# Kernel tuning notes

Measured on AMD Instinct MI355X. Metric: run time of the kernel, lower is better.

Reference implementation:

```python
import jax, jax.numpy as jnp
import numpy as np

N_NODES = 100000
N_EDGES = 3200000
IN_DIM, H_DIM, OUT_DIM = 512, 256, 128
NEG_SLOPE = 0.25


def setup_inputs() -> dict:
    key = jax.random.key(0)
    ks = jax.random.split(key, 8)
    x = jax.random.normal(ks[0], (N_NODES, IN_DIM), dtype=jnp.float32)
    # xavier-normal-ish init for weights, zero bias (matches module init)
    W1 = jax.random.normal(ks[1], (IN_DIM, H_DIM), dtype=jnp.float32) * np.sqrt(2.0 / (IN_DIM + H_DIM))
    b1 = jnp.zeros((H_DIM,), dtype=jnp.float32)
    W2 = jax.random.normal(ks[2], (H_DIM, OUT_DIM), dtype=jnp.float32) * np.sqrt(2.0 / (H_DIM + OUT_DIM))
    b2 = jnp.zeros((OUT_DIM,), dtype=jnp.float32)
    adj_row = jax.random.randint(ks[3], (N_EDGES,), 0, N_NODES, dtype=jnp.int32)
    adj_col = jax.random.randint(ks[4], (N_EDGES,), 0, N_NODES, dtype=jnp.int32)
    # positive normalized-ish edge weights (like D^-1/2 A D^-1/2 entries)
    edge_weight = jax.random.uniform(ks[5], (N_EDGES,), dtype=jnp.float32) * 0.05
    return {"x": x, "W1": W1, "b1": b1, "W2": W2, "b2": b2,
            "adj_row": adj_row, "adj_col": adj_col, "edge_weight": edge_weight}


def reference(x, W1, b1, W2, b2, adj_row, adj_col, edge_weight):
    n = x.shape[0]

    def spmm(support):
        # out[r] = sum over edges (r, c): w * support[c]   (COO SpMM)
        msgs = edge_weight[:, None] * support[adj_col]  # [E, d] gather
        return jax.ops.segment_sum(msgs, adj_row, num_segments=n)

    def leaky(h):
        return jnp.where(h > 0, h, NEG_SLOPE * h)

    h = leaky(spmm(x @ W1) + b1)          # gc1 + leaky_relu (dropout = eval mode)
    h = leaky(spmm(h @ W2) + b2)          # gc2 + leaky_relu
    return h
```

## Files before the change

kernel.cpp:

```cpp
#include <hip/hip_runtime.h>

typedef unsigned short u16;
typedef unsigned char u8;
typedef __attribute__((ext_vector_type(8))) __bf16 bf16x8;
typedef __attribute__((ext_vector_type(4))) float f32x4;

#define CAP   4608
#define CAPO  5504
#define CHUNK 8192
#define NBKT_PAD 800

static __device__ __forceinline__ u16 f2bf(float f) {
    return __builtin_bit_cast(u16, (__bf16)f);
}
static __device__ __forceinline__ void gl_lds16(const void* g, void* l) {
    __builtin_amdgcn_global_load_lds((const __attribute__((address_space(1))) void*)g,
                                     (__attribute__((address_space(3))) void*)l, 16, 0, 0);
}


__global__ __launch_bounds__(256) void bucket_k(const int* __restrict__ row,
                                                const int* __restrict__ col,
                                                const float* __restrict__ w,
                                                int* __restrict__ gcount,
                                                int2* __restrict__ edges, int E) {
    __shared__ int hist[NBKT_PAD];
    __shared__ int lscan[NBKT_PAD];
    __shared__ int lcnt[NBKT_PAD];
    __shared__ int gbase[NBKT_PAD];
    __shared__ int tsum[256];
    __shared__ int2 pay[CHUNK];
    __shared__ int  dst[CHUNK];
    const int base = blockIdx.x * CHUNK;
    const int cntC = min(CHUNK, E - base);
    const int tid = threadIdx.x;

    for (int i = tid; i < NBKT_PAD; i += 256) { hist[i] = 0; lcnt[i] = 0; }
    __syncthreads();

    for (int i = tid; i < cntC; i += 256) atomicAdd(&hist[row[base + i] >> 7], 1);
    __syncthreads();

    int h[4], s = 0;
    #pragma unroll
    for (int j = 0; j < 4; ++j) {
        int bb = tid * 4 + j;
        h[j] = (bb < NBKT_PAD) ? hist[bb] : 0;
        s += h[j];
    }
    tsum[tid] = s;
    __syncthreads();
    for (int d = 1; d < 256; d <<= 1) {
        int t = (tid >= d) ? tsum[tid - d] : 0;
        __syncthreads();
        tsum[tid] += t;
        __syncthreads();
    }
    int run = tsum[tid] - s;
    #pragma unroll
    for (int j = 0; j < 4; ++j) {
        int bb = tid * 4 + j;
        if (bb < NBKT_PAD) {
            lscan[bb] = run;
            run += h[j];
            if (h[j] > 0) gbase[bb] = atomicAdd(&gcount[bb], h[j]);
        }
    }
    __syncthreads();

    for (int i = tid; i < cntC; i += 256) {
        int r = row[base + i];
        int c = col[base + i];
        float ww = w[base + i];
        int bb = r >> 7;
        int lp = atomicAdd(&lcnt[bb], 1);
        int slot = lscan[bb] + lp;
        int pos = gbase[bb] + lp;
        pay[slot] = make_int2(((r & 127) << 17) | c, __float_as_int(ww));
        dst[slot] = (pos < CAP) ? bb * CAP + pos : -1;
    }
    __syncthreads();

    for (int i = tid; i < cntC; i += 256) {
        int d = dst[i];
        if (d >= 0) edges[d] = pay[i];
    }
}


__global__ __launch_bounds__(256) void rsort_k(const int* __restrict__ gcount,
                                               const int2* __restrict__ edges,
                                               int* __restrict__ colsO,
                                               float* __restrict__ wO,
                                               int2* __restrict__ rc, int n, int nbkt) {
    __shared__ int hist[128];
    __shared__ int sbase[128];
    __shared__ int lcnt[128];
    __shared__ int sc[128];
    __shared__ int colsL[CAPO];
    __shared__ float wL[CAPO];
    const int b = blockIdx.x, tid = threadIdx.x;
    const int cnt = min(gcount[b], CAP);
    const int2* eb = edges + (size_t)b * CAP;

    if (tid < 128) { hist[tid] = 0; lcnt[tid] = 0; }
    for (int i = tid; i < CAPO; i += 256) { colsL[i] = 0; wL[i] = 0.f; }
    __syncthreads();

    for (int i = tid; i < cnt; i += 256) atomicAdd(&hist[((unsigned)eb[i].x) >> 17], 1);
    __syncthreads();

    int hp = 0;
    if (tid < 128) { hp = (hist[tid] + 7) & ~7; sc[tid] = hp; }
    __syncthreads();
    for (int d = 1; d < 128; d <<= 1) {
        int t = 0;
        if (tid < 128 && tid >= d) t = sc[tid - d];
        __syncthreads();
        if (tid < 128) sc[tid] += t;
        __syncthreads();
    }
    if (tid < 128) {
        int start = sc[tid] - hp;
        sbase[tid] = start;
        int gr = b * 128 + tid;
        if (gr < n) rc[gr] = make_int2(b * CAPO + start, hp);
    }
    __syncthreads();

    for (int i = tid; i < cnt; i += 256) {
        int2 e = eb[i];
        int rr = ((unsigned)e.x) >> 17;
        int slot = sbase[rr] + atomicAdd(&lcnt[rr], 1);
        colsL[slot] = (e.x & 0x1FFFF) << 8;
        wL[slot] = __int_as_float(e.y);
    }
    __syncthreads();

    int* co = colsO + (size_t)b * CAPO;
    float* wo = wO + (size_t)b * CAPO;
    for (int i = tid; i < CAPO; i += 256) { co[i] = colsL[i]; wo[i] = wL[i]; }
    if (b == nbkt - 1 && tid < 64) {
        colsO[(size_t)nbkt * CAPO + tid] = 0;
        wO[(size_t)nbkt * CAPO + tid] = 0.f;
    }
}


__global__ __launch_bounds__(256) void wscale_k(const int* __restrict__ cols,
                                                const float* __restrict__ wr,
                                                const float* __restrict__ scales,
                                                float* __restrict__ ws, int total) {
    int i = (blockIdx.x * 256 + threadIdx.x) * 4;
    const int stride = gridDim.x * 1024;
    for (; i < total; i += stride) {
        int4 c = *(const int4*)(cols + i);
        float4 w = *(const float4*)(wr + i);
        float4 o;
        o.x = w.x * scales[((unsigned)c.x) >> 8];
        o.y = w.y * scales[((unsigned)c.y) >> 8];
        o.z = w.z * scales[((unsigned)c.z) >> 8];
        o.w = w.w * scales[((unsigned)c.w) >> 8];
        *(float4*)(ws + i) = o;
    }
}


__global__ void transpose_w2(const float* __restrict__ W1, u16* __restrict__ W1T,
                             const float* __restrict__ W2, u16* __restrict__ W2T,
                             int* __restrict__ gcount) {
    const int T1 = 512 * 256;
    const int T2 = 256 * 128;
    int i = blockIdx.x * blockDim.x + threadIdx.x;
    if (i < NBKT_PAD) gcount[i] = 0;
    if (i < T1) {
        int k = i / 256, nn = i % 256;
        W1T[nn * 512 + k] = f2bf(W1[i]);
    } else if (i < T1 + T2) {
        int j = i - T1;
        int k = j / 128, nn = j % 128;
        W2T[nn * 256 + k] = f2bf(W2[j]);
    }
}


template <int K, int NWN, bool AF32>
__global__ void gemm_fq(const void* __restrict__ Ap,
                        const u16* __restrict__ BT,
                        u8* __restrict__ supq,
                        float* __restrict__ scales, int M) {
    constexpr int BN = NWN * 64;
    constexpr int THREADS = NWN * 128;
    constexpr int A_ISS = 8192 / (THREADS * 16);
    constexpr int B_ISS = (BN * 64) / (THREADS * 16);
    constexpr int LOGN = (NWN == 4) ? 2 : 1;
    static_assert(!AF32 || (4096 / (THREADS * 8)) == 1, "AF32 path assumes A_CH==1");
    __shared__ alignas(16) u16 As[128 * 32];
    __shared__ alignas(16) u16 Bs[BN * 32];
    __shared__ float rmax[128][NWN];
    __shared__ u8 qtile[128 * BN];

    const int tid = threadIdx.x;
    const int lane = tid & 63, wv = tid >> 6;
    const int wm = wv >> LOGN, wn = wv & (NWN - 1);
    const int lr = lane & 15, lg = lane >> 4;
    const int mblk = blockIdx.x;
    f32x4 acc[4][4] = {};
    const float* Af = (const float*)Ap;
    const u16* Ab = (const u16*)Ap;

    const u16* gB[B_ISS];
    u16* lB[B_ISS];
    #pragma unroll
    for (int i = 0; i < B_ISS; ++i) {
        int t8 = i * THREADS + tid;
        gB[i] = BT + (long)(t8 >> 2) * K + (t8 & 3) * 8;
        lB[i] = Bs + i * THREADS * 8 + wv * 512;
    }

    if constexpr (AF32) {
        long r = (long)mblk * 128 + (tid >> 2);
        if (r >= M) r = M - 1;
        const float* gAf0 = Af + r * K + (tid & 3) * 8;
        u16* lAf0 = As + (tid >> 2) * 32 + (tid & 3) * 8;

        float4 pf0 = *(const float4*)(gAf0 + 0);
        float4 pf1 = *(const float4*)(gAf0 + 4);
        #pragma unroll 4
        for (int kt = 0; kt < K; kt += 32) {
            #pragma unroll
            for (int i = 0; i < B_ISS; ++i) gl_lds16(gB[i] + kt, lB[i]);
            __builtin_amdgcn_sched_barrier(0);
            const int ktn = (kt + 32 < K) ? kt + 32 : 0;
            float4 nf0 = *(const float4*)(gAf0 + ktn);
            float4 nf1 = *(const float4*)(gAf0 + ktn + 4);
            bf16x8 t;
            t[0] = (__bf16)pf0.x; t[1] = (__bf16)pf0.y; t[2] = (__bf16)pf0.z; t[3] = (__bf16)pf0.w;
            t[4] = (__bf16)pf1.x; t[5] = (__bf16)pf1.y; t[6] = (__bf16)pf1.z; t[7] = (__bf16)pf1.w;
            *(bf16x8*)lAf0 = t;
            asm volatile("s_waitcnt vmcnt(2) lgkmcnt(0)" ::: "memory");
            __builtin_amdgcn_sched_barrier(0);
            __builtin_amdgcn_s_barrier();
            __builtin_amdgcn_sched_barrier(0);

            bf16x8 a[4], b[4];
            #pragma unroll
            for (int mi = 0; mi < 4; ++mi)
                a[mi] = *(const bf16x8*)&As[(wm * 64 + mi * 16 + lr) * 32 + lg * 8];
            #pragma unroll
            for (int ni = 0; ni < 4; ++ni)
                b[ni] = *(const bf16x8*)&Bs[(wn * 64 + ni * 16 + lr) * 32 + lg * 8];
            #pragma unroll
            for (int mi = 0; mi < 4; ++mi)
                #pragma unroll
                for (int ni = 0; ni < 4; ++ni)
                    acc[mi][ni] = __builtin_amdgcn_mfma_f32_16x16x32_bf16(a[mi], b[ni], acc[mi][ni], 0, 0, 0);
            __builtin_amdgcn_sched_barrier(0);
            __builtin_amdgcn_s_barrier();
            __builtin_amdgcn_sched_barrier(0);
            pf0 = nf0; pf1 = nf1;
        }
    } else {
        const u16* gA[A_ISS];
        u16* lA[A_ISS];
        #pragma unroll
        for (int i = 0; i < A_ISS; ++i) {
            int t8 = i * THREADS + tid;
            long r = (long)mblk * 128 + (t8 >> 2);
            if (r >= M) r = M - 1;
            gA[i] = Ab + r * K + (t8 & 3) * 8;
            lA[i] = As + i * THREADS * 8 + wv * 512;
        }
        #pragma unroll 2
        for (int kt = 0; kt < K; kt += 32) {
            #pragma unroll
            for (int i = 0; i < A_ISS; ++i) gl_lds16(gA[i] + kt, lA[i]);
            #pragma unroll
            for (int i = 0; i < B_ISS; ++i) gl_lds16(gB[i] + kt, lB[i]);
            __syncthreads();

            bf16x8 a[4], b[4];
            #pragma unroll
            for (int mi = 0; mi < 4; ++mi)
                a[mi] = *(const bf16x8*)&As[(wm * 64 + mi * 16 + lr) * 32 + lg * 8];
            #pragma unroll
            for (int ni = 0; ni < 4; ++ni)
                b[ni] = *(const bf16x8*)&Bs[(wn * 64 + ni * 16 + lr) * 32 + lg * 8];
            #pragma unroll
            for (int mi = 0; mi < 4; ++mi)
                #pragma unroll
                for (int ni = 0; ni < 4; ++ni)
                    acc[mi][ni] = __builtin_amdgcn_mfma_f32_16x16x32_bf16(a[mi], b[ni], acc[mi][ni], 0, 0, 0);
            __syncthreads();
        }
    }

    #pragma unroll
    for (int mi = 0; mi < 4; ++mi) {
        #pragma unroll
        for (int j = 0; j < 4; ++j) {
            float m = 0.f;
            #pragma unroll
            for (int ni = 0; ni < 4; ++ni) m = fmaxf(m, fabsf(acc[mi][ni][j]));
            m = fmaxf(m, __shfl_xor(m, 1));
            m = fmaxf(m, __shfl_xor(m, 2));
            m = fmaxf(m, __shfl_xor(m, 4));
            m = fmaxf(m, __shfl_xor(m, 8));
            if (lr == 0) rmax[wm * 64 + mi * 16 + lg * 4 + j][wn] = m;
        }
    }
    __syncthreads();

    #pragma unroll
    for (int mi = 0; mi < 4; ++mi) {
        #pragma unroll
        for (int j = 0; j < 4; ++j) {
            const int rl = wm * 64 + mi * 16 + lg * 4 + j;
            float m = rmax[rl][0];
            #pragma unroll
            for (int w2 = 1; w2 < NWN; ++w2) m = fmaxf(m, rmax[rl][w2]);
            const float inv = (m > 0.f) ? 127.f / m : 0.f;
            #pragma unroll
            for (int ni = 0; ni < 4; ++ni) {
                int q = (int)rintf(acc[mi][ni][j] * inv) + 128;
                qtile[rl * BN + wn * 64 + ni * 16 + lr] = (u8)q;
            }
        }
    }
    if (tid < 128) {
        int gr = mblk * 128 + tid;
        if (gr < M) {
            float m = rmax[tid][0];
            #pragma unroll
            for (int w2 = 1; w2 < NWN; ++w2) m = fmaxf(m, rmax[tid][w2]);
            scales[gr] = m * (1.f / 127.f);
        }
    }
    __syncthreads();

    constexpr int CHUNKS = (128 * BN) / (THREADS * 16);
    #pragma unroll
    for (int cc = 0; cc < CHUNKS; ++cc) {
        int off = cc * THREADS * 16 + tid * 16;
        int gr = mblk * 128 + off / BN;
        if (gr < M)
            *(int4*)(supq + (size_t)mblk * 128 * BN + off) = *(const int4*)&qtile[off];
    }
}


__global__ __launch_bounds__(256) void spmm_l1(const int2* __restrict__ rc,
                                               const int* __restrict__ cols,
                                               const float* __restrict__ ws,
                                               const u8* __restrict__ supq,
                                               const float* __restrict__ bias,
                                               u16* __restrict__ obf, int n) {
    const int r = blockIdx.x * 4 + (threadIdx.x >> 6);
    if (r >= n) return;
    const int lane = threadIdx.x & 63;
    const int half = lane >> 5;
    const unsigned lsub8 = (unsigned)(lane & 31) * 8;
    float acc[8] = {0.f, 0.f, 0.f, 0.f, 0.f, 0.f, 0.f, 0.f};
    float kk = 0.f;
    const int2 se = rc[r];
    const int e0  = __builtin_amdgcn_readfirstlane(se.x);
    const int cnt = __builtin_amdgcn_readfirstlane(se.y);
    const int* __restrict__ cp = cols + e0;
    const float* __restrict__ wp = ws + e0;

#define L1_ISSUE(G0, G1, G2, G3, IDX) {                                              \
    int4 ca = *(const int4*)(cp + (IDX));                                            \
    int4 cb = *(const int4*)(cp + (IDX) + 4);                                        \
    G0 = *(const uint2*)(supq + ((unsigned)(half ? ca.y : ca.x) + lsub8));           \
    G1 = *(const uint2*)(supq + ((unsigned)(half ? ca.w : ca.z) + lsub8));           \
    G2 = *(const uint2*)(supq + ((unsigned)(half ? cb.y : cb.x) + lsub8));           \
    G3 = *(const uint2*)(supq + ((unsigned)(half ? cb.w : cb.z) + lsub8)); }

#define L1_PAIR(WX, WY, G) {                                                         \
    const float wsel = half ? (WY) : (WX);                                           \
    kk += wsel;                                                                      \
    acc[0] += wsel * (float)((G).x & 0xFF);                                          \
    acc[1] += wsel * (float)(((G).x >> 8) & 0xFF);                                   \
    acc[2] += wsel * (float)(((G).x >> 16) & 0xFF);                                  \
    acc[3] += wsel * (float)((G).x >> 24);                                           \
    acc[4] += wsel * (float)((G).y & 0xFF);                                          \
    acc[5] += wsel * (float)(((G).y >> 8) & 0xFF);                                   \
    acc[6] += wsel * (float)(((G).y >> 16) & 0xFF);                                  \
    acc[7] += wsel * (float)((G).y >> 24); }

#define L1_CONSUME(G0, G1, G2, G3, IDX) {                                            \
    float4 wa = *(const float4*)(wp + (IDX));                                        \
    float4 wb = *(const float4*)(wp + (IDX) + 4);                                    \
    L1_PAIR(wa.x, wa.y, G0) L1_PAIR(wa.z, wa.w, G1)                                  \
    L1_PAIR(wb.x, wb.y, G2) L1_PAIR(wb.z, wb.w, G3) }

    if (cnt > 0) {
        uint2 a0, a1, a2, a3, b0, b1, b2, b3, c0, c1, c2, c3, d0, d1, d2, d3;
        L1_ISSUE(a0, a1, a2, a3, 0)
        if (8 < cnt)  L1_ISSUE(b0, b1, b2, b3, 8)
        if (16 < cnt) L1_ISSUE(c0, c1, c2, c3, 16)
        if (24 < cnt) L1_ISSUE(d0, d1, d2, d3, 24)
        int i = 0;
        while (i + 32 < cnt) {
            L1_CONSUME(a0, a1, a2, a3, i)
            L1_ISSUE(a0, a1, a2, a3, i + 32)
            L1_CONSUME(b0, b1, b2, b3, i + 8)
            if (i + 40 < cnt) L1_ISSUE(b0, b1, b2, b3, i + 40)
            L1_CONSUME(c0, c1, c2, c3, i + 16)
            if (i + 48 < cnt) L1_ISSUE(c0, c1, c2, c3, i + 48)
            L1_CONSUME(d0, d1, d2, d3, i + 24)
            if (i + 56 < cnt) L1_ISSUE(d0, d1, d2, d3, i + 56)
            i += 32;
        }
        if (i < cnt)      L1_CONSUME(a0, a1, a2, a3, i)
        if (i + 8 < cnt)  L1_CONSUME(b0, b1, b2, b3, i + 8)
        if (i + 16 < cnt) L1_CONSUME(c0, c1, c2, c3, i + 16)
        if (i + 24 < cnt) L1_CONSUME(d0, d1, d2, d3, i + 24)
    }
#undef L1_ISSUE
#undef L1_PAIR
#undef L1_CONSUME

    kk += __shfl_xor(kk, 32);
    #pragma unroll
    for (int j = 0; j < 8; ++j) acc[j] += __shfl_xor(acc[j], 32);

    const float off = 128.f * kk;
    float a0 = half ? acc[4] : acc[0];
    float a1 = half ? acc[5] : acc[1];
    float a2 = half ? acc[6] : acc[2];
    float a3 = half ? acc[7] : acc[3];
    const int d0 = (lane & 31) * 8 + half * 4;
    const float4 bb = *(const float4*)&bias[d0];
    float h0 = a0 - off + bb.x, h1 = a1 - off + bb.y;
    float h2 = a2 - off + bb.z, h3 = a3 - off + bb.w;
    h0 = h0 > 0.f ? h0 : 0.25f * h0;
    h1 = h1 > 0.f ? h1 : 0.25f * h1;
    h2 = h2 > 0.f ? h2 : 0.25f * h2;
    h3 = h3 > 0.f ? h3 : 0.25f * h3;
    ushort4 hv; hv.x = f2bf(h0); hv.y = f2bf(h1); hv.z = f2bf(h2); hv.w = f2bf(h3);
    *(ushort4*)&obf[(size_t)r * 256 + d0] = hv;
}


__global__ __launch_bounds__(256) void spmm_l2(const int2* __restrict__ rc,
                                               const int* __restrict__ cols,
                                               const float* __restrict__ ws,
                                               const u8* __restrict__ supq,
                                               const float* __restrict__ bias,
                                               float* __restrict__ of32, int n) {
    const int r = blockIdx.x * 4 + (threadIdx.x >> 6);
    if (r >= n) return;
    const int lane = threadIdx.x & 63;
    const int quad = lane >> 4;
    const unsigned lsub8 = (unsigned)(lane & 15) * 8;
    float acc[8] = {0.f, 0.f, 0.f, 0.f, 0.f, 0.f, 0.f, 0.f};
    float kk = 0.f;
    const int2 se = rc[r];
    const int e0  = __builtin_amdgcn_readfirstlane(se.x);
    const int cnt = __builtin_amdgcn_readfirstlane(se.y);
    const int* __restrict__ cp = cols + e0;
    const float* __restrict__ wp = ws + e0;

#define L2_SELI(CA) ((quad & 2) ? ((quad & 1) ? (CA).w : (CA).z) : ((quad & 1) ? (CA).y : (CA).x))
#define L2_SELF(WA) ((quad & 2) ? ((quad & 1) ? (WA).w : (WA).z) : ((quad & 1) ? (WA).y : (WA).x))

#define L2_ISSUE(G0, G1, IDX) {                                                      \
    int4 ca = *(const int4*)(cp + (IDX));                                            \
    int4 cb = *(const int4*)(cp + (IDX) + 4);                                        \
    G0 = *(const uint2*)(supq + ((((unsigned)L2_SELI(ca)) >> 1) + lsub8));           \
    G1 = *(const uint2*)(supq + ((((unsigned)L2_SELI(cb)) >> 1) + lsub8)); }

#define L2_QUAD(WSEL, G) {                                                           \
    kk += WSEL;                                                                      \
    acc[0] += WSEL * (float)((G).x & 0xFF);                                          \
    acc[1] += WSEL * (float)(((G).x >> 8) & 0xFF);                                   \
    acc[2] += WSEL * (float)(((G).x >> 16) & 0xFF);                                  \
    acc[3] += WSEL * (float)((G).x >> 24);                                           \
    acc[4] += WSEL * (float)((G).y & 0xFF);                                          \
    acc[5] += WSEL * (float)(((G).y >> 8) & 0xFF);                                   \
    acc[6] += WSEL * (float)(((G).y >> 16) & 0xFF);                                  \
    acc[7] += WSEL * (float)((G).y >> 24); }

#define L2_CONSUME(G0, G1, IDX) {                                                    \
    float4 wa = *(const float4*)(wp + (IDX));                                        \
    float4 wb = *(const float4*)(wp + (IDX) + 4);                                    \
    const float wsa = L2_SELF(wa);                                                   \
    const float wsb = L2_SELF(wb);                                                   \
    L2_QUAD(wsa, G0) L2_QUAD(wsb, G1) }

    if (cnt > 0) {
        uint2 a0, a1, b0, b1, c0, c1, d0, d1;
        L2_ISSUE(a0, a1, 0)
        if (8 < cnt)  L2_ISSUE(b0, b1, 8)
        if (16 < cnt) L2_ISSUE(c0, c1, 16)
        if (24 < cnt) L2_ISSUE(d0, d1, 24)
        int i = 0;
        while (i + 32 < cnt) {
            L2_CONSUME(a0, a1, i)
            L2_ISSUE(a0, a1, i + 32)
            L2_CONSUME(b0, b1, i + 8)
            if (i + 40 < cnt) L2_ISSUE(b0, b1, i + 40)
            L2_CONSUME(c0, c1, i + 16)
            if (i + 48 < cnt) L2_ISSUE(c0, c1, i + 48)
            L2_CONSUME(d0, d1, i + 24)
            if (i + 56 < cnt) L2_ISSUE(d0, d1, i + 56)
            i += 32;
        }
        if (i < cnt)      L2_CONSUME(a0, a1, i)
        if (i + 8 < cnt)  L2_CONSUME(b0, b1, i + 8)
        if (i + 16 < cnt) L2_CONSUME(c0, c1, i + 16)
        if (i + 24 < cnt) L2_CONSUME(d0, d1, i + 24)
    }
#undef L2_ISSUE
#undef L2_QUAD
#undef L2_CONSUME
#undef L2_SELI
#undef L2_SELF

    kk += __shfl_xor(kk, 16);
    kk += __shfl_xor(kk, 32);
    #pragma unroll
    for (int j = 0; j < 8; ++j) {
        acc[j] += __shfl_xor(acc[j], 16);
        acc[j] += __shfl_xor(acc[j], 32);
    }

    const float off = 128.f * kk;
    float a0 = (quad & 2) ? ((quad & 1) ? acc[6] : acc[4]) : ((quad & 1) ? acc[2] : acc[0]);
    float a1 = (quad & 2) ? ((quad & 1) ? acc[7] : acc[5]) : ((quad & 1) ? acc[3] : acc[1]);
    const int d0 = (lane & 15) * 8 + quad * 2;
    const float2 bb = *(const float2*)&bias[d0];
    float h0 = a0 - off + bb.x, h1 = a1 - off + bb.y;
    h0 = h0 > 0.f ? h0 : 0.25f * h0;
    h1 = h1 > 0.f ? h1 : 0.25f * h1;
    *(float2*)&of32[(size_t)r * 128 + d0] = make_float2(h0, h1);
}


extern "C" void kernel_launch(void* const* d_in, const int* in_sizes, int n_in,
                              void* d_out, int out_size, void* d_ws, size_t ws_size,
                              hipStream_t stream) {
    const float* x  = (const float*)d_in[0];
    const float* W1 = (const float*)d_in[1];
    const float* b1 = (const float*)d_in[2];
    const float* W2 = (const float*)d_in[3];
    const float* b2 = (const float*)d_in[4];
    const int* arow = (const int*)d_in[5];
    const int* acol = (const int*)d_in[6];
    const float* ew = (const float*)d_in[7];

    const int IN = 512, H = 256, OUT = 128;
    const int n = in_sizes[0] / IN;
    const int E = in_sizes[5];
    const int nbkt = (n + 127) >> 7;
    const int totS = nbkt * CAPO;
    const int totS2 = totS + 64;

    char* base = (char*)d_ws;
    size_t off = 0;
    auto carve = [&](size_t bytes) -> void* {
        void* r = base + off;
        off = (off + bytes + 255) & ~(size_t)255;
        return r;
    };
    int*   gcount = (int*)carve((size_t)NBKT_PAD * 4);
    int2*  edges  = (int2*)carve((size_t)nbkt * CAP * 8);
    int*   colsS  = (int*)carve((size_t)totS2 * 4);
    float* wraw   = (float*)carve((size_t)totS2 * 4);
    float* wsS    = (float*)carve((size_t)totS2 * 4);
    int2*  rc     = (int2*)carve((size_t)n * 8);
    u16*   W1T    = (u16*)carve((size_t)H * IN * 2);
    u16*   W2T    = (u16*)carve((size_t)OUT * H * 2);
    u8*    supq   = (u8*)carve((size_t)n * H);
    float* scales = (float*)carve((size_t)n * 4);
    u16*   h1     = (u16*)carve((size_t)n * H * 2);

    transpose_w2<<<(512 * 256 + 256 * 128 + 255) / 256, 256, 0, stream>>>(W1, W1T, W2, W2T, gcount);

    bucket_k<<<(E + CHUNK - 1) / CHUNK, 256, 0, stream>>>(arow, acol, ew, gcount, edges, E);
    rsort_k<<<nbkt, 256, 0, stream>>>(gcount, edges, colsS, wraw, rc, n, nbkt);

    gemm_fq<512, 4, true><<<(n + 127) / 128, 512, 0, stream>>>(x, W1T, supq, scales, n);
    wscale_k<<<(totS2 / 4 + 255) / 256, 256, 0, stream>>>(colsS, wraw, scales, wsS, totS2);
    spmm_l1<<<(n + 3) / 4, 256, 0, stream>>>(rc, colsS, wsS, supq, b1, h1, n);

    gemm_fq<256, 2, false><<<(n + 127) / 128, 256, 0, stream>>>(h1, W2T, supq, scales, n);
    wscale_k<<<(totS2 / 4 + 255) / 256, 256, 0, stream>>>(colsS, wraw, scales, wsS, totS2);
    spmm_l2<<<(n + 3) / 4, 256, 0, stream>>>(rc, colsS, wsS, supq, b2, (float*)d_out, n);
}
```

Measured before the change: 470.6 us.

## Fuse weight transpose into bucketing and co-schedule row sort with layer-1 GEMM

The weight transpose/bf16 conversion is merged into the edge bucketing kernel as extra blocks, and gcount zeroing moves to a memset. The row-sort and the layer-1 GEMM now run as one kernel that interleaves the two roles across alternating blocks through shared memory, so the sparse sort can overlap the dense GEMM. The bucketing chunk is halved to give more blocks. This cuts launches and idle tails, but the fused kernel allocates the larger shared-memory footprint and 512 threads for every block, which may lower occupancy for the sort blocks.

New measurement: 506.7 us. 7.7% more time.

```diff
diff --git a/kernel.cpp b/kernel.cpp
--- a/kernel.cpp
+++ b/kernel.cpp
@@ -7,7 +7,7 @@
 
 #define CAP   4608
 #define CAPO  5504
-#define CHUNK 8192
+#define CHUNK 4096
 #define NBKT_PAD 800
 
 static __device__ __forceinline__ u16 f2bf(float f) {
@@ -19,11 +19,27 @@
 }
 
 
-__global__ __launch_bounds__(256) void bucket_k(const int* __restrict__ row,
-                                                const int* __restrict__ col,
-                                                const float* __restrict__ w,
-                                                int* __restrict__ gcount,
-                                                int2* __restrict__ edges, int E) {
+__global__ __launch_bounds__(256) void prep_k(const int* __restrict__ row,
+                                              const int* __restrict__ col,
+                                              const float* __restrict__ w,
+                                              int* __restrict__ gcount,
+                                              int2* __restrict__ edges, int E, int nbb,
+                                              const float* __restrict__ W1, u16* __restrict__ W1T,
+                                              const float* __restrict__ W2, u16* __restrict__ W2T) {
+    const int tid = threadIdx.x;
+    if ((int)blockIdx.x >= nbb) {
+        const int T1 = 512 * 256, T2 = 256 * 128;
+        int i = ((int)blockIdx.x - nbb) * 256 + tid;
+        if (i < T1) {
+            int k = i / 256, nn = i % 256;
+            W1T[nn * 512 + k] = f2bf(W1[i]);
+        } else if (i < T1 + T2) {
+            int j = i - T1;
+            int k = j / 128, nn = j % 128;
+            W2T[nn * 256 + k] = f2bf(W2[j]);
+        }
+        return;
+    }
     __shared__ int hist[NBKT_PAD];
     __shared__ int lscan[NBKT_PAD];
     __shared__ int lcnt[NBKT_PAD];
@@ -33,7 +49,6 @@
     __shared__ int  dst[CHUNK];
     const int base = blockIdx.x * CHUNK;
     const int cntC = min(CHUNK, E - base);
-    const int tid = threadIdx.x;
 
     for (int i = tid; i < NBKT_PAD; i += 256) { hist[i] = 0; lcnt[i] = 0; }
     __syncthreads();
@@ -88,26 +103,26 @@
 }
 
 
-__global__ __launch_bounds__(256) void rsort_k(const int* __restrict__ gcount,
-                                               const int2* __restrict__ edges,
-                                               int* __restrict__ colsO,
-                                               float* __restrict__ wO,
-                                               int2* __restrict__ rc, int n, int nbkt) {
-    __shared__ int hist[128];
-    __shared__ int sbase[128];
-    __shared__ int lcnt[128];
-    __shared__ int sc[128];
-    __shared__ int colsL[CAPO];
-    __shared__ float wL[CAPO];
-    const int b = blockIdx.x, tid = threadIdx.x;
+static __device__ void rsort_core(char* smem, int b, const int* __restrict__ gcount,
+                                  const int2* __restrict__ edges,
+                                  int* __restrict__ colsO, float* __restrict__ wO,
+                                  int2* __restrict__ rc, int n, int nbkt) {
+    int* hist  = (int*)smem;
+    int* sbase = hist + 128;
+    int* lcnt  = sbase + 128;
+    int* sc    = lcnt + 128;
+    int* colsL = sc + 128;
+    float* wL  = (float*)(colsL + CAPO);
+    const int tid = threadIdx.x;
+    const int NT = blockDim.x;
     const int cnt = min(gcount[b], CAP);
     const int2* eb = edges + (size_t)b * CAP;
 
     if (tid < 128) { hist[tid] = 0; lcnt[tid] = 0; }
-    for (int i = tid; i < CAPO; i += 256) { colsL[i] = 0; wL[i] = 0.f; }
-    __syncthreads();
-
-    for (int i = tid; i < cnt; i += 256) atomicAdd(&hist[((unsigned)eb[i].x) >> 17], 1);
+    for (int i = tid; i < CAPO; i += NT) { colsL[i] = 0; wL[i] = 0.f; }
+    __syncthreads();
+
+    for (int i = tid; i < cnt; i += NT) atomicAdd(&hist[((unsigned)eb[i].x) >> 17], 1);
     __syncthreads();
 
     int hp = 0;
@@ -128,7 +143,7 @@
     }
     __syncthreads();
 
-    for (int i = tid; i < cnt; i += 256) {
+    for (int i = tid; i < cnt; i += NT) {
         int2 e = eb[i];
         int rr = ((unsigned)e.x) >> 17;
         int slot = sbase[rr] + atomicAdd(&lcnt[rr], 1);
@@ -139,11 +154,200 @@
 
     int* co = colsO + (size_t)b * CAPO;
     float* wo = wO + (size_t)b * CAPO;
-    for (int i = tid; i < CAPO; i += 256) { co[i] = colsL[i]; wo[i] = wL[i]; }
+    for (int i = tid; i < CAPO; i += NT) { co[i] = colsL[i]; wo[i] = wL[i]; }
     if (b == nbkt - 1 && tid < 64) {
         colsO[(size_t)nbkt * CAPO + tid] = 0;
         wO[(size_t)nbkt * CAPO + tid] = 0.f;
     }
+}
+
+
+template <int K, int NWN, bool AF32>
+static __device__ void gemm_core(char* smem, int mblk, const void* __restrict__ Ap,
+                                 const u16* __restrict__ BT,
+                                 u8* __restrict__ supq, float* __restrict__ scales, int M) {
+    constexpr int BN = NWN * 64;
+    constexpr int THREADS = NWN * 128;
+    constexpr int A_ISS = 8192 / (THREADS * 16);
+    constexpr int B_ISS = (BN * 64) / (THREADS * 16);
+    constexpr int LOGN = (NWN == 4) ? 2 : 1;
+    static_assert(!AF32 || (4096 / (THREADS * 8)) == 1, "AF32 path assumes A_CH==1");
+    u16* As = (u16*)smem;
+    u16* Bs = (u16*)(smem + 8192);
+    float* rmax = (float*)(smem + 8192 + NWN * 4096);
+    u8* qtile = (u8*)(smem + 8192 + NWN * 4096 + 512 * NWN);
+
+    const int tid = threadIdx.x;
+    const int lane = tid & 63, wv = tid >> 6;
+    const int wm = wv >> LOGN, wn = wv & (NWN - 1);
+    const int lr = lane & 15, lg = lane >> 4;
+    f32x4 acc[4][4] = {};
+    const float* Af = (const float*)Ap;
+    const u16* Ab = (const u16*)Ap;
+
+    const u16* gB[B_ISS];
+    u16* lB[B_ISS];
+    #pragma unroll
+    for (int i = 0; i < B_ISS; ++i) {
+        int t8 = i * THREADS + tid;
+        gB[i] = BT + (long)(t8 >> 2) * K + (t8 & 3) * 8;
+        lB[i] = Bs + i * THREADS * 8 + wv * 512;
+    }
+
+    if constexpr (AF32) {
+        long r = (long)mblk * 128 + (tid >> 2);
+        if (r >= M) r = M - 1;
+        const float* gAf0 = Af + r * K + (tid & 3) * 8;
+        u16* lAf0 = As + (tid >> 2) * 32 + (tid & 3) * 8;
+
+        float4 pf0 = *(const float4*)(gAf0 + 0);
+        float4 pf1 = *(const float4*)(gAf0 + 4);
+        #pragma unroll 4
+        for (int kt = 0; kt < K; kt += 32) {
+            #pragma unroll
+            for (int i = 0; i < B_ISS; ++i) gl_lds16(gB[i] + kt, lB[i]);
+            __builtin_amdgcn_sched_barrier(0);
+            const int ktn = (kt + 32 < K) ? kt + 32 : 0;
+            float4 nf0 = *(const float4*)(gAf0 + ktn);
+            float4 nf1 = *(const float4*)(gAf0 + ktn + 4);
+            bf16x8 t;
+            t[0] = (__bf16)pf0.x; t[1] = (__bf16)pf0.y; t[2] = (__bf16)pf0.z; t[3] = (__bf16)pf0.w;
+            t[4] = (__bf16)pf1.x; t[5] = (__bf16)pf1.y; t[6] = (__bf16)pf1.z; t[7] = (__bf16)pf1.w;
+            *(bf16x8*)lAf0 = t;
+            asm volatile("s_waitcnt vmcnt(2) lgkmcnt(0)" ::: "memory");
+            __builtin_amdgcn_sched_barrier(0);
+            __builtin_amdgcn_s_barrier();
+            __builtin_amdgcn_sched_barrier(0);
+
+            bf16x8 a[4], b[4];
+            #pragma unroll
+            for (int mi = 0; mi < 4; ++mi)
+                a[mi] = *(const bf16x8*)&As[(wm * 64 + mi * 16 + lr) * 32 + lg * 8];
+            #pragma unroll
+            for (int ni = 0; ni < 4; ++ni)
+                b[ni] = *(const bf16x8*)&Bs[(wn * 64 + ni * 16 + lr) * 32 + lg * 8];
+            #pragma unroll
+            for (int mi = 0; mi < 4; ++mi)
+                #pragma unroll
+                for (int ni = 0; ni < 4; ++ni)
+                    acc[mi][ni] = __builtin_amdgcn_mfma_f32_16x16x32_bf16(a[mi], b[ni], acc[mi][ni], 0, 0, 0);
+            __builtin_amdgcn_sched_barrier(0);
+            __builtin_amdgcn_s_barrier();
+            __builtin_amdgcn_sched_barrier(0);
+            pf0 = nf0; pf1 = nf1;
+        }
+    } else {
+        const u16* gA[A_ISS];
+        u16* lA[A_ISS];
+        #pragma unroll
+        for (int i = 0; i < A_ISS; ++i) {
+            int t8 = i * THREADS + tid;
+            long r = (long)mblk * 128 + (t8 >> 2);
+            if (r >= M) r = M - 1;
+            gA[i] = Ab + r * K + (t8 & 3) * 8;
+            lA[i] = As + i * THREADS * 8 + wv * 512;
+        }
+        #pragma unroll 2
+        for (int kt = 0; kt < K; kt += 32) {
+            #pragma unroll
+            for (int i = 0; i < A_ISS; ++i) gl_lds16(gA[i] + kt, lA[i]);
+            #pragma unroll
+            for (int i = 0; i < B_ISS; ++i) gl_lds16(gB[i] + kt, lB[i]);
+            __syncthreads();
+
+            bf16x8 a[4], b[4];
+            #pragma unroll
+            for (int mi = 0; mi < 4; ++mi)
+                a[mi] = *(const bf16x8*)&As[(wm * 64 + mi * 16 + lr) * 32 + lg * 8];
+            #pragma unroll
+            for (int ni = 0; ni < 4; ++ni)
+                b[ni] = *(const bf16x8*)&Bs[(wn * 64 + ni * 16 + lr) * 32 + lg * 8];
+            #pragma unroll
+            for (int mi = 0; mi < 4; ++mi)
+                #pragma unroll
+                for (int ni = 0; ni < 4; ++ni)
+                    acc[mi][ni] = __builtin_amdgcn_mfma_f32_16x16x32_bf16(a[mi], b[ni], acc[mi][ni], 0, 0, 0);
+            __syncthreads();
+        }
+    }
+
+    #pragma unroll
+    for (int mi = 0; mi < 4; ++mi) {
+        #pragma unroll
+        for (int j = 0; j < 4; ++j) {
+            float m = 0.f;
+            #pragma unroll
+            for (int ni = 0; ni < 4; ++ni) m = fmaxf(m, fabsf(acc[mi][ni][j]));
+            m = fmaxf(m, __shfl_xor(m, 1));
+            m = fmaxf(m, __shfl_xor(m, 2));
+            m = fmaxf(m, __shfl_xor(m, 4));
+            m = fmaxf(m, __shfl_xor(m, 8));
+            if (lr == 0) rmax[(wm * 64 + mi * 16 + lg * 4 + j) * NWN + wn] = m;
+        }
+    }
+    __syncthreads();
+
+    #pragma unroll
+    for (int mi = 0; mi < 4; ++mi) {
+        #pragma unroll
+        for (int j = 0; j < 4; ++j) {
+            const int rl = wm * 64 + mi * 16 + lg * 4 + j;
+            float m = rmax[rl * NWN];
+            #pragma unroll
+            for (int w2 = 1; w2 < NWN; ++w2) m = fmaxf(m, rmax[rl * NWN + w2]);
+            const float inv = (m > 0.f) ? 127.f / m : 0.f;
+            #pragma unroll
+            for (int ni = 0; ni < 4; ++ni) {
+                int q = (int)rintf(acc[mi][ni][j] * inv) + 128;
+                qtile[rl * BN + wn * 64 + ni * 16 + lr] = (u8)q;
+            }
+        }
+    }
+    if (tid < 128) {
+        int gr = mblk * 128 + tid;
+        if (gr < M) {
+            float m = rmax[tid * NWN];
+            #pragma unroll
+            for (int w2 = 1; w2 < NWN; ++w2) m = fmaxf(m, rmax[tid * NWN + w2]);
+            scales[gr] = m * (1.f / 127.f);
+        }
+    }
+    __syncthreads();
+
+    constexpr int CHUNKS = (128 * BN) / (THREADS * 16);
+    #pragma unroll
+    for (int cc = 0; cc < CHUNKS; ++cc) {
+        int off = cc * THREADS * 16 + tid * 16;
+        int gr = mblk * 128 + off / BN;
+        if (gr < M)
+            *(int4*)(supq + (size_t)mblk * 128 * BN + off) = *(const int4*)&qtile[off];
+    }
+}
+
+
+__global__ __launch_bounds__(512) void mid_k(const float* __restrict__ x,
+                                             const u16* __restrict__ W1T,
+                                             u8* __restrict__ supq, float* __restrict__ scales,
+                                             const int* __restrict__ gcount,
+                                             const int2* __restrict__ edges,
+                                             int* __restrict__ colsS, float* __restrict__ wraw,
+                                             int2* __restrict__ rc, int n, int nbkt) {
+    __shared__ alignas(16) char smem[59392];
+    const int idx = blockIdx.x >> 1;
+    if (blockIdx.x & 1) {
+        rsort_core(smem, idx, gcount, edges, colsS, wraw, rc, n, nbkt);
+    } else {
+        gemm_core<512, 4, true>(smem, idx, x, W1T, supq, scales, n);
+    }
+}
+
+
+__global__ __launch_bounds__(256) void gemm2_k(const u16* __restrict__ h1,
+                                               const u16* __restrict__ W2T,
+                                               u8* __restrict__ supq,
+                                               float* __restrict__ scales, int M) {
+    __shared__ alignas(16) char smem[33792];
+    gemm_core<256, 2, false>(smem, blockIdx.x, h1, W2T, supq, scales, M);
 }
 
 
@@ -162,189 +366,6 @@
         o.z = w.z * scales[((unsigned)c.z) >> 8];
         o.w = w.w * scales[((unsigned)c.w) >> 8];
         *(float4*)(ws + i) = o;
-    }
-}
-
-
-__global__ void transpose_w2(const float* __restrict__ W1, u16* __restrict__ W1T,
-                             const float* __restrict__ W2, u16* __restrict__ W2T,
-                             int* __restrict__ gcount) {
-    const int T1 = 512 * 256;
-    const int T2 = 256 * 128;
-    int i = blockIdx.x * blockDim.x + threadIdx.x;
-    if (i < NBKT_PAD) gcount[i] = 0;
-    if (i < T1) {
-        int k = i / 256, nn = i % 256;
-        W1T[nn * 512 + k] = f2bf(W1[i]);
-    } else if (i < T1 + T2) {
-        int j = i - T1;
-        int k = j / 128, nn = j % 128;
-        W2T[nn * 256 + k] = f2bf(W2[j]);
-    }
-}
-
-
-template <int K, int NWN, bool AF32>
-__global__ void gemm_fq(const void* __restrict__ Ap,
-                        const u16* __restrict__ BT,
-                        u8* __restrict__ supq,
-                        float* __restrict__ scales, int M) {
-    constexpr int BN = NWN * 64;
-    constexpr int THREADS = NWN * 128;
-    constexpr int A_ISS = 8192 / (THREADS * 16);
-    constexpr int B_ISS = (BN * 64) / (THREADS * 16);
-    constexpr int LOGN = (NWN == 4) ? 2 : 1;
-    static_assert(!AF32 || (4096 / (THREADS * 8)) == 1, "AF32 path assumes A_CH==1");
-    __shared__ alignas(16) u16 As[128 * 32];
-    __shared__ alignas(16) u16 Bs[BN * 32];
-    __shared__ float rmax[128][NWN];
-    __shared__ u8 qtile[128 * BN];
-
-    const int tid = threadIdx.x;
-    const int lane = tid & 63, wv = tid >> 6;
-    const int wm = wv >> LOGN, wn = wv & (NWN - 1);
-    const int lr = lane & 15, lg = lane >> 4;
-    const int mblk = blockIdx.x;
-    f32x4 acc[4][4] = {};
-    const float* Af = (const float*)Ap;
-    const u16* Ab = (const u16*)Ap;
-
-    const u16* gB[B_ISS];
-    u16* lB[B_ISS];
-    #pragma unroll
-    for (int i = 0; i < B_ISS; ++i) {
-        int t8 = i * THREADS + tid;
-        gB[i] = BT + (long)(t8 >> 2) * K + (t8 & 3) * 8;
-        lB[i] = Bs + i * THREADS * 8 + wv * 512;
-    }
-
-    if constexpr (AF32) {
-        long r = (long)mblk * 128 + (tid >> 2);
-        if (r >= M) r = M - 1;
-        const float* gAf0 = Af + r * K + (tid & 3) * 8;
-        u16* lAf0 = As + (tid >> 2) * 32 + (tid & 3) * 8;
-
-        float4 pf0 = *(const float4*)(gAf0 + 0);
-        float4 pf1 = *(const float4*)(gAf0 + 4);
-        #pragma unroll 4
-        for (int kt = 0; kt < K; kt += 32) {
-            #pragma unroll
-            for (int i = 0; i < B_ISS; ++i) gl_lds16(gB[i] + kt, lB[i]);
-            __builtin_amdgcn_sched_barrier(0);
-            const int ktn = (kt + 32 < K) ? kt + 32 : 0;
-            float4 nf0 = *(const float4*)(gAf0 + ktn);
-            float4 nf1 = *(const float4*)(gAf0 + ktn + 4);
-            bf16x8 t;
-            t[0] = (__bf16)pf0.x; t[1] = (__bf16)pf0.y; t[2] = (__bf16)pf0.z; t[3] = (__bf16)pf0.w;
-            t[4] = (__bf16)pf1.x; t[5] = (__bf16)pf1.y; t[6] = (__bf16)pf1.z; t[7] = (__bf16)pf1.w;
-            *(bf16x8*)lAf0 = t;
-            asm volatile("s_waitcnt vmcnt(2) lgkmcnt(0)" ::: "memory");
-            __builtin_amdgcn_sched_barrier(0);
-            __builtin_amdgcn_s_barrier();
-            __builtin_amdgcn_sched_barrier(0);
-
-            bf16x8 a[4], b[4];
-            #pragma unroll
-            for (int mi = 0; mi < 4; ++mi)
-                a[mi] = *(const bf16x8*)&As[(wm * 64 + mi * 16 + lr) * 32 + lg * 8];
-            #pragma unroll
-            for (int ni = 0; ni < 4; ++ni)
-                b[ni] = *(const bf16x8*)&Bs[(wn * 64 + ni * 16 + lr) * 32 + lg * 8];
-            #pragma unroll
-            for (int mi = 0; mi < 4; ++mi)
-                #pragma unroll
-                for (int ni = 0; ni < 4; ++ni)
-                    acc[mi][ni] = __builtin_amdgcn_mfma_f32_16x16x32_bf16(a[mi], b[ni], acc[mi][ni], 0, 0, 0);
-            __builtin_amdgcn_sched_barrier(0);
-            __builtin_amdgcn_s_barrier();
-            __builtin_amdgcn_sched_barrier(0);
-            pf0 = nf0; pf1 = nf1;
-        }
-    } else {
-        const u16* gA[A_ISS];
-        u16* lA[A_ISS];
-        #pragma unroll
-        for (int i = 0; i < A_ISS; ++i) {
-            int t8 = i * THREADS + tid;
-            long r = (long)mblk * 128 + (t8 >> 2);
-            if (r >= M) r = M - 1;
-            gA[i] = Ab + r * K + (t8 & 3) * 8;
-            lA[i] = As + i * THREADS * 8 + wv * 512;
-        }
-        #pragma unroll 2
-        for (int kt = 0; kt < K; kt += 32) {
-            #pragma unroll
-            for (int i = 0; i < A_ISS; ++i) gl_lds16(gA[i] + kt, lA[i]);
-            #pragma unroll
-            for (int i = 0; i < B_ISS; ++i) gl_lds16(gB[i] + kt, lB[i]);
-            __syncthreads();
-
-            bf16x8 a[4], b[4];
-            #pragma unroll
-            for (int mi = 0; mi < 4; ++mi)
-                a[mi] = *(const bf16x8*)&As[(wm * 64 + mi * 16 + lr) * 32 + lg * 8];
-            #pragma unroll
-            for (int ni = 0; ni < 4; ++ni)
-                b[ni] = *(const bf16x8*)&Bs[(wn * 64 + ni * 16 + lr) * 32 + lg * 8];
-            #pragma unroll
-            for (int mi = 0; mi < 4; ++mi)
-                #pragma unroll
-                for (int ni = 0; ni < 4; ++ni)
-                    acc[mi][ni] = __builtin_amdgcn_mfma_f32_16x16x32_bf16(a[mi], b[ni], acc[mi][ni], 0, 0, 0);
-            __syncthreads();
-        }
-    }
-
-    #pragma unroll
-    for (int mi = 0; mi < 4; ++mi) {
-        #pragma unroll
-        for (int j = 0; j < 4; ++j) {
-            float m = 0.f;
-            #pragma unroll
-            for (int ni = 0; ni < 4; ++ni) m = fmaxf(m, fabsf(acc[mi][ni][j]));
-            m = fmaxf(m, __shfl_xor(m, 1));
-            m = fmaxf(m, __shfl_xor(m, 2));
-            m = fmaxf(m, __shfl_xor(m, 4));
-            m = fmaxf(m, __shfl_xor(m, 8));
-            if (lr == 0) rmax[wm * 64 + mi * 16 + lg * 4 + j][wn] = m;
-        }
-    }
-    __syncthreads();
-
-    #pragma unroll
-    for (int mi = 0; mi < 4; ++mi) {
-        #pragma unroll
-        for (int j = 0; j < 4; ++j) {
-            const int rl = wm * 64 + mi * 16 + lg * 4 + j;
-            float m = rmax[rl][0];
-            #pragma unroll
-            for (int w2 = 1; w2 < NWN; ++w2) m = fmaxf(m, rmax[rl][w2]);
-            const float inv = (m > 0.f) ? 127.f / m : 0.f;
-            #pragma unroll
-            for (int ni = 0; ni < 4; ++ni) {
-                int q = (int)rintf(acc[mi][ni][j] * inv) + 128;
-                qtile[rl * BN + wn * 64 + ni * 16 + lr] = (u8)q;
-            }
-        }
-    }
-    if (tid < 128) {
-        int gr = mblk * 128 + tid;
-        if (gr < M) {
-            float m = rmax[tid][0];
-            #pragma unroll
-            for (int w2 = 1; w2 < NWN; ++w2) m = fmaxf(m, rmax[tid][w2]);
-            scales[gr] = m * (1.f / 127.f);
-        }
-    }
-    __syncthreads();
-
-    constexpr int CHUNKS = (128 * BN) / (THREADS * 16);
-    #pragma unroll
-    for (int cc = 0; cc < CHUNKS; ++cc) {
-        int off = cc * THREADS * 16 + tid * 16;
-        int gr = mblk * 128 + off / BN;
-        if (gr < M)
-            *(int4*)(supq + (size_t)mblk * 128 * BN + off) = *(const int4*)&qtile[off];
     }
 }
 
@@ -554,6 +575,7 @@
     const int n = in_sizes[0] / IN;
     const int E = in_sizes[5];
     const int nbkt = (n + 127) >> 7;
+    const int nbb = (E + CHUNK - 1) / CHUNK;
     const int totS = nbkt * CAPO;
     const int totS2 = totS + 64;
 
@@ -576,16 +598,19 @@
     float* scales = (float*)carve((size_t)n * 4);
     u16*   h1     = (u16*)carve((size_t)n * H * 2);
 
-    transpose_w2<<<(512 * 256 + 256 * 128 + 255) / 256, 256, 0, stream>>>(W1, W1T, W2, W2T, gcount);
-
-    bucket_k<<<(E + CHUNK - 1) / CHUNK, 256, 0, stream>>>(arow, acol, ew, gcount, edges, E);
-    rsort_k<<<nbkt, 256, 0, stream>>>(gcount, edges, colsS, wraw, rc, n, nbkt);
-
-    gemm_fq<512, 4, true><<<(n + 127) / 128, 512, 0, stream>>>(x, W1T, supq, scales, n);
+    hipMemsetAsync(gcount, 0, (size_t)NBKT_PAD * 4, stream);
+
+    const int tblocks = (IN * H + H * OUT + 255) / 256;
+    prep_k<<<nbb + tblocks, 256, 0, stream>>>(arow, acol, ew, gcount, edges, E, nbb,
+                                              W1, W1T, W2, W2T);
+
+    mid_k<<<2 * nbkt, 512, 0, stream>>>(x, W1T, supq, scales, gcount, edges,
+                                        colsS, wraw, rc, n, nbkt);
+
     wscale_k<<<(totS2 / 4 + 255) / 256, 256, 0, stream>>>(colsS, wraw, scales, wsS, totS2);
     spmm_l1<<<(n + 3) / 4, 256, 0, stream>>>(rc, colsS, wsS, supq, b1, h1, n);
 
-    gemm_fq<256, 2, false><<<(n + 127) / 128, 256, 0, stream>>>(h1, W2T, supq, scales, n);
+    gemm2_k<<<nbkt, 256, 0, stream>>>(h1, W2T, supq, scales, n);
     wscale_k<<<(totS2 / 4 + 255) / 256, 256, 0, stream>>>(colsS, wraw, scales, wsS, totS2);
     spmm_l2<<<(n + 3) / 4, 256, 0, stream>>>(rc, colsS, wsS, supq, b2, (float*)d_out, n);
 }
```
